# Kernel optimization log

Hardware: AMD Instinct MI355X
Metric: run time of the kernel (lower is better)

Reference implementation:

```python
import jax, jax.numpy as jnp
import numpy as np


def setup_inputs() -> dict:
    key = jax.random.key(0)
    k1, k2, k3 = jax.random.split(key, 3)
    B, C, T = 8, 256, 4096
    H, K = 512, 4
    x = jax.random.normal(k1, (B, C, T), dtype=jnp.float32)
    W = jax.random.normal(k2, (H, C * K), dtype=jnp.float32) * 0.02
    b = jax.random.normal(k3, (H,), dtype=jnp.float32) * 0.02
    return {"x": x, "W": W, "b": b}


def reference(x, W, b):
    # Causal conv1d equivalent of the per-step Linear loop (stride=1).
    # Original flattens window as view(B, C*K): channel-major -> W[h, c*K + k].
    B, C, T = x.shape
    H = W.shape[0]
    K = W.shape[1] // C
    kernel = W.reshape(H, C, K)  # OIH layout
    out = jax.lax.conv_general_dilated(
        x, kernel,
        window_strides=(1,),
        padding=[(K - 1, 0)],  # left-pad only => causal
        dimension_numbers=("NCH", "OIH", "NCH"),
    )
    return out + b[None, :, None]  # (B, H, T)
```

## Files before the change

kernel.cpp:

```cpp
#include <hip/hip_runtime.h>
#include <hip/hip_bf16.h>


#define Bb 8
#define Cc 256
#define Tt 4096
#define Hh 512
#define Kk 4

typedef __attribute__((ext_vector_type(8))) short bf16x8;
typedef __attribute__((ext_vector_type(4))) float f32x4;

#define WS_XT_OFF   0
#define WS_WT_OFF   16777216
#define WS_ZERO_OFF 17825792
#define WS_NEEDED   17826816ULL

__device__ __forceinline__ void gload16(const void* g, void* l) {
    __builtin_amdgcn_global_load_lds(
        (const __attribute__((address_space(1))) void*)g,
        (__attribute__((address_space(3))) void*)l, 16, 0, 0);
}

__global__ __launch_bounds__(256) void prep_kernel(const float* __restrict__ x,
                                                   const float* __restrict__ W,
                                                   __hip_bfloat16* __restrict__ xT,
                                                   __hip_bfloat16* __restrict__ Wt,
                                                   float* __restrict__ zeros) {
    __shared__ __hip_bfloat16 tile[64][72];
    const int bid = blockIdx.x;
    if (bid < 2048) {
        const int t0 = (bid & 63) * 64, c0 = ((bid >> 6) & 3) * 64, b = bid >> 8;
        const int lt = threadIdx.x & 63, lw = threadIdx.x >> 6;
#pragma unroll
        for (int i = 0; i < 16; ++i) {
            int cc = lw + i * 4;
            tile[cc][lt] = __float2bfloat16(x[((size_t)(b * Cc + c0 + cc)) * Tt + t0 + lt]);
        }
        __syncthreads();
#pragma unroll
        for (int i = 0; i < 2; ++i) {
            int tt = (threadIdx.x >> 3) + i * 32;
            int c8 = threadIdx.x & 7;
            short tmp[8];
#pragma unroll
            for (int j = 0; j < 8; ++j) {
                __hip_bfloat16 v = tile[c8 * 8 + j][tt];
                tmp[j] = *reinterpret_cast<short*>(&v);
            }
            *reinterpret_cast<bf16x8*>(&xT[((size_t)(b * Tt + t0 + tt)) * Cc + c0 + c8 * 8]) =
                *reinterpret_cast<bf16x8*>(tmp);
        }
    } else {
        int n = (bid - 2048) * 256 + threadIdx.x;
        int c = n & 255;
        int h = (n >> 8) & 511;
        int k = n >> 17;
        Wt[n] = __float2bfloat16(W[h * (Cc * Kk) + c * Kk + k]);
        if (bid == 2048) zeros[threadIdx.x] = 0.f;
    }
}

#define A_BUF    16384
#define B_BUF    9216
#define B_BASE   32768
#define LDS_TOTAL 51200

#define BAR __builtin_amdgcn_s_barrier()
#define LGKM0 do { asm volatile("s_waitcnt lgkmcnt(0)" ::: "memory"); \
                   __builtin_amdgcn_sched_barrier(0); } while (0)

__global__ __launch_bounds__(256, 3) void conv_mfma_kernel(
    const __hip_bfloat16* __restrict__ xT,
    const __hip_bfloat16* __restrict__ Wt,
    const float* __restrict__ bias,
    const float* __restrict__ zeros,
    float* __restrict__ out)
{
    __shared__ __align__(1024) char smem[LDS_TOTAL];
    const int tid = threadIdx.x, lane = tid & 63, wave = tid >> 6;
    const int wr = wave >> 1, wc = wave & 1;
    const int l15 = lane & 15, lg = lane >> 4;

    const int flat = blockIdx.x + 32 * blockIdx.y + 128 * blockIdx.z;
    const int nf   = (flat & 7) * 128 + (flat >> 3);
    const int h0 = (nf & 3) * 128;
    const int t0 = ((nf >> 2) & 31) * 128;
    const int b  = nf >> 7;

    const char* Wt_c = (const char*)Wt;
    const char* xT_c = (const char*)xT;
    const char* zz   = (const char*)zeros;

    const char* asrc[4]; int adst_[4];
#pragma unroll
    for (int i = 0; i < 4; ++i) {
        int s = tid + i * 256;
        int kk = s >> 9, row = (s >> 2) & 127, sl = s & 3;
        int colch = (sl ^ ((row >> 1) & 3)) * 8;
        asrc[i] = Wt_c + (((size_t)(kk * Hh + h0 + row)) * Cc + colch) * 2;
        adst_[i] = s * 16;
    }
    const char* bsrc[3]; int bdst_[3]; int bstep[3];
#pragma unroll
    for (int i = 0; i < 3; ++i) {
        int s = (i < 2) ? tid + i * 256 : 512 + lane;
        int row = s >> 2, sl = s & 3;
        int colch = (sl ^ ((row >> 1) & 3)) * 8;
        int tg = t0 - 3 + row;
        bool valid = (row <= 130) && (tg >= 0);
        bsrc[i]  = valid ? xT_c + (((size_t)b * Tt + tg) * Cc + colch) * 2
                         : zz + (s & 15) * 16;
        bstep[i] = valid ? 64 : 0;
        bdst_[i] = s * 16;
    }

    const int aoffb = (wr * 64 + l15) * 64 + ((lg ^ ((l15 >> 1) & 3)) << 4);
    int btab[4];
#pragma unroll
    for (int k = 0; k < 4; ++k)
        btab[k] = (wc * 64 + l15 + k) * 64 + ((lg ^ (((l15 + k) >> 1) & 3)) << 4);

    f32x4 acc[4][4] = {};

#pragma unroll
    for (int i = 0; i < 4; ++i) gload16(asrc[i], smem + adst_[i]);
#pragma unroll
    for (int i = 0; i < 2; ++i) gload16(bsrc[i], smem + B_BASE + bdst_[i]);
    if (wave == 0) gload16(bsrc[2], smem + B_BASE + bdst_[2]);
    asm volatile("s_waitcnt vmcnt(0)" ::: "memory");
    BAR;

#pragma unroll
    for (int s = 0; s < 16; ++s) {
        const int p  = s >> 1;
        const int kb = 2 * (s & 1);
        const char* Ab = smem + (s & 1) * A_BUF;
        const char* Bbf = smem + B_BASE + (p & 1) * B_BUF;

        if (s < 15) {
            const long aadv = (long)((s + 1) & 1) * 524288 + (long)((s + 1) >> 1) * 64;
            char* An = smem + ((s + 1) & 1) * A_BUF;
#pragma unroll
            for (int i = 0; i < 4; ++i) gload16(asrc[i] + aadv, An + adst_[i]);
        }
        if (((s & 1) == 0) && (p < 7)) {
            char* Bn = smem + B_BASE + ((p + 1) & 1) * B_BUF;
#pragma unroll
            for (int i = 0; i < 2; ++i) gload16(bsrc[i] + (p + 1) * bstep[i], Bn + bdst_[i]);
            if (wave == 0) gload16(bsrc[2] + (p + 1) * bstep[2], Bn + bdst_[2]);
        }

        bf16x8 a_[4], b_[4];
#pragma unroll
        for (int fm = 0; fm < 4; ++fm) a_[fm] = *(const bf16x8*)(Ab + aoffb + fm * 1024);
#pragma unroll
        for (int ft = 0; ft < 4; ++ft) b_[ft] = *(const bf16x8*)(Bbf + btab[kb] + ft * 1024);
        LGKM0;
        __builtin_amdgcn_s_setprio(1);
#pragma unroll
        for (int fm = 0; fm < 4; ++fm)
#pragma unroll
            for (int ft = 0; ft < 4; ++ft)
                acc[fm][ft] = __builtin_amdgcn_mfma_f32_16x16x32_bf16(a_[fm], b_[ft], acc[fm][ft], 0, 0, 0);
        __builtin_amdgcn_s_setprio(0);
#pragma unroll
        for (int fm = 0; fm < 4; ++fm) a_[fm] = *(const bf16x8*)(Ab + 8192 + aoffb + fm * 1024);
#pragma unroll
        for (int ft = 0; ft < 4; ++ft) b_[ft] = *(const bf16x8*)(Bbf + btab[kb + 1] + ft * 1024);
        LGKM0;
        __builtin_amdgcn_s_setprio(1);
#pragma unroll
        for (int fm = 0; fm < 4; ++fm)
#pragma unroll
            for (int ft = 0; ft < 4; ++ft)
                acc[fm][ft] = __builtin_amdgcn_mfma_f32_16x16x32_bf16(a_[fm], b_[ft], acc[fm][ft], 0, 0, 0);
        __builtin_amdgcn_s_setprio(0);

        if (s < 15) {
            if (((s & 1) == 0) && (p < 7)) asm volatile("s_waitcnt vmcnt(3)" ::: "memory");
            else                           asm volatile("s_waitcnt vmcnt(0)" ::: "memory");
            BAR;
        }
    }

#pragma unroll
    for (int fm = 0; fm < 4; ++fm) {
        int hb = h0 + wr * 64 + fm * 16 + lg * 4;
        float4 bs = *(const float4*)&bias[hb];
        const float* bsp = (const float*)&bs;
#pragma unroll
        for (int q = 0; q < 4; ++q)
#pragma unroll
            for (int ft = 0; ft < 4; ++ft) {
                int t = t0 + wc * 64 + ft * 16 + l15;
                out[((size_t)(b * Hh + hb + q)) * Tt + t] = acc[fm][ft][q] + bsp[q];
            }
    }
}

#define TT 256
#define HT 8
#define CT 4
__global__ __launch_bounds__(256) void conv1d_f32_kernel(
    const float* __restrict__ x, const float* __restrict__ W,
    const float* __restrict__ bias, float* __restrict__ out)
{
    const int tid = threadIdx.x;
    const int t0 = blockIdx.x * TT;
    const int h0 = blockIdx.y * HT;
    const int b  = blockIdx.z;
    __shared__ float xs[CT][TT + Kk];
    float acc[HT];
#pragma unroll
    for (int h = 0; h < HT; ++h) acc[h] = 0.f;
    const float* xb = x + (size_t)b * Cc * Tt;
    for (int c0 = 0; c0 < Cc; c0 += CT) {
        __syncthreads();
#pragma unroll
        for (int cc = 0; cc < CT; ++cc)
            for (int j = tid; j < TT + Kk - 1; j += 256) {
                int idx = t0 - (Kk - 1) + j;
                xs[cc][j] = (idx >= 0) ? xb[(size_t)(c0 + cc) * Tt + idx] : 0.f;
            }
        __syncthreads();
#pragma unroll
        for (int cc = 0; cc < CT; ++cc) {
            float xv[Kk];
#pragma unroll
            for (int k = 0; k < Kk; ++k) xv[k] = xs[cc][tid + k];
#pragma unroll
            for (int h = 0; h < HT; ++h) {
                const float* wp = W + (size_t)(h0 + h) * (Cc * Kk) + (size_t)(c0 + cc) * Kk;
#pragma unroll
                for (int k = 0; k < Kk; ++k) acc[h] += wp[k] * xv[k];
            }
        }
    }
#pragma unroll
    for (int h = 0; h < HT; ++h)
        out[((size_t)b * Hh + (h0 + h)) * Tt + t0 + tid] = acc[h] + bias[h0 + h];
}

extern "C" void kernel_launch(void* const* d_in, const int* in_sizes, int n_in,
                              void* d_out, int out_size, void* d_ws, size_t ws_size,
                              hipStream_t stream) {
    const float* x    = (const float*)d_in[0];
    const float* W    = (const float*)d_in[1];
    const float* bias = (const float*)d_in[2];
    float* out        = (float*)d_out;

    if (ws_size >= WS_NEEDED) {
        __hip_bfloat16* xT = (__hip_bfloat16*)((char*)d_ws + WS_XT_OFF);
        __hip_bfloat16* Wt = (__hip_bfloat16*)((char*)d_ws + WS_WT_OFF);
        float* zeros       = (float*)((char*)d_ws + WS_ZERO_OFF);

        prep_kernel<<<dim3(4096), dim3(256), 0, stream>>>(x, W, xT, Wt, zeros);
        conv_mfma_kernel<<<dim3(32, 4, 8), dim3(256), 0, stream>>>(xT, Wt, bias, zeros, out);
    } else {
        conv1d_f32_kernel<<<dim3(Tt / TT, Hh / HT, Bb), dim3(256), 0, stream>>>(x, W, bias, out);
    }
}
```

Measured before the change: 49.91 us.

## Switch to 32x32x16 MFMA tiles and triple-buffer the weight tiles

The GEMM inner loop now uses 32x32x16 bf16 MFMA instructions with a 2x2 fragment grid per wave, replacing the 4x4 grid of 16x16x32 instructions. This cuts the number of LDS fragment reads per unit of math. The weight (A) operand moves from double to triple buffering in LDS so that loads are issued two stages ahead, with the vmcnt waits adjusted to match. The larger LDS footprint drops the occupancy target from 3 to 2 blocks per CU. The loop is only unrolled by 2, and all waves now issue the third B load, which duplicates a write to the same LDS addresses.

```diff
diff --git a/kernel.cpp b/kernel.cpp
--- a/kernel.cpp
+++ b/kernel.cpp
@@ -8,8 +8,8 @@
 #define Hh 512
 #define Kk 4
 
-typedef __attribute__((ext_vector_type(8))) short bf16x8;
-typedef __attribute__((ext_vector_type(4))) float f32x4;
+typedef __attribute__((ext_vector_type(8)))  short bf16x8;
+typedef __attribute__((ext_vector_type(16))) float f32x16;
 
 #define WS_XT_OFF   0
 #define WS_WT_OFF   16777216
@@ -63,14 +63,14 @@
 
 #define A_BUF    16384
 #define B_BUF    9216
-#define B_BASE   32768
-#define LDS_TOTAL 51200
+#define B_BASE   49152
+#define LDS_TOTAL 67584
 
 #define BAR __builtin_amdgcn_s_barrier()
 #define LGKM0 do { asm volatile("s_waitcnt lgkmcnt(0)" ::: "memory"); \
                    __builtin_amdgcn_sched_barrier(0); } while (0)
 
-__global__ __launch_bounds__(256, 3) void conv_mfma_kernel(
+__global__ __launch_bounds__(256, 2) void conv_mfma_kernel(
     const __hip_bfloat16* __restrict__ xT,
     const __hip_bfloat16* __restrict__ Wt,
     const float* __restrict__ bias,
@@ -80,7 +80,7 @@
     __shared__ __align__(1024) char smem[LDS_TOTAL];
     const int tid = threadIdx.x, lane = tid & 63, wave = tid >> 6;
     const int wr = wave >> 1, wc = wave & 1;
-    const int l15 = lane & 15, lg = lane >> 4;
+    const int l31 = lane & 31, lh = lane >> 5;
 
     const int flat = blockIdx.x + 32 * blockIdx.y + 128 * blockIdx.z;
     const int nf   = (flat & 7) * 128 + (flat >> 3);
@@ -115,88 +115,99 @@
         bdst_[i] = s * 16;
     }
 
-    const int aoffb = (wr * 64 + l15) * 64 + ((lg ^ ((l15 >> 1) & 3)) << 4);
-    int btab[4];
-#pragma unroll
-    for (int k = 0; k < 4; ++k)
-        btab[k] = (wc * 64 + l15 + k) * 64 + ((lg ^ (((l15 + k) >> 1) & 3)) << 4);
-
-    f32x4 acc[4][4] = {};
-
-#pragma unroll
-    for (int i = 0; i < 4; ++i) gload16(asrc[i], smem + adst_[i]);
-#pragma unroll
-    for (int i = 0; i < 2; ++i) gload16(bsrc[i], smem + B_BASE + bdst_[i]);
-    if (wave == 0) gload16(bsrc[2], smem + B_BASE + bdst_[2]);
-    asm volatile("s_waitcnt vmcnt(0)" ::: "memory");
+    int arow[2], aswz[2];
+#pragma unroll
+    for (int fm = 0; fm < 2; ++fm) {
+        int r = wr * 64 + fm * 32 + l31;
+        arow[fm] = r * 64; aswz[fm] = (r >> 1) & 3;
+    }
+    int brow[4][2], bswz[4][2];
+#pragma unroll
+    for (int ck = 0; ck < 4; ++ck)
+#pragma unroll
+        for (int ft = 0; ft < 2; ++ft) {
+            int r = wc * 64 + ft * 32 + l31 + ck;
+            brow[ck][ft] = r * 64; bswz[ck][ft] = (r >> 1) & 3;
+        }
+
+    f32x16 acc[2][2] = {};
+
+    int A0 = 0, A1 = A_BUF, A2 = 2 * A_BUF;
+    int Bc = B_BASE, Bn = B_BASE + B_BUF;
+
+#pragma unroll
+    for (int i = 0; i < 4; ++i) gload16(asrc[i], smem + A0 + adst_[i]);
+#pragma unroll
+    for (int i = 0; i < 3; ++i) gload16(bsrc[i], smem + Bc + bdst_[i]);
+#pragma unroll
+    for (int i = 0; i < 4; ++i) gload16(asrc[i] + 524288, smem + A1 + adst_[i]);
+    asm volatile("s_waitcnt vmcnt(4)" ::: "memory");
     BAR;
 
-#pragma unroll
+#pragma unroll 2
     for (int s = 0; s < 16; ++s) {
-        const int p  = s >> 1;
-        const int kb = 2 * (s & 1);
-        const char* Ab = smem + (s & 1) * A_BUF;
-        const char* Bbf = smem + B_BASE + (p & 1) * B_BUF;
+        const int kb = (s & 1) * 2;
+
+        if (s <= 13) {
+            const long aadv = (long)((s + 2) & 1) * 524288 + (long)((s + 2) >> 1) * 64;
+#pragma unroll
+            for (int i = 0; i < 4; ++i) gload16(asrc[i] + aadv, smem + A2 + adst_[i]);
+        }
+        if (((s & 1) == 0) && (s <= 12)) {
+            const int bu = (s >> 1) + 1;
+#pragma unroll
+            for (int i = 0; i < 3; ++i) gload16(bsrc[i] + bu * bstep[i], smem + Bn + bdst_[i]);
+        }
+
+#pragma unroll
+        for (int kk = 0; kk < 2; ++kk) {
+            const int ck = kb + kk;
+            bf16x8 a_[2][2], b_[2][2];
+#pragma unroll
+            for (int sub = 0; sub < 2; ++sub) {
+#pragma unroll
+                for (int fm = 0; fm < 2; ++fm)
+                    a_[sub][fm] = *(const bf16x8*)(smem + A0 + kk * 8192 + arow[fm]
+                                    + (((sub * 2 + lh) ^ aswz[fm]) << 4));
+#pragma unroll
+                for (int ft = 0; ft < 2; ++ft)
+                    b_[sub][ft] = *(const bf16x8*)(smem + Bc + brow[ck][ft]
+                                    + (((sub * 2 + lh) ^ bswz[ck][ft]) << 4));
+            }
+            LGKM0;
+            __builtin_amdgcn_s_setprio(1);
+#pragma unroll
+            for (int sub = 0; sub < 2; ++sub)
+#pragma unroll
+                for (int fm = 0; fm < 2; ++fm)
+#pragma unroll
+                    for (int ft = 0; ft < 2; ++ft)
+                        acc[fm][ft] = __builtin_amdgcn_mfma_f32_32x32x16_bf16(
+                            a_[sub][fm], b_[sub][ft], acc[fm][ft], 0, 0, 0);
+            __builtin_amdgcn_s_setprio(0);
+        }
 
         if (s < 15) {
-            const long aadv = (long)((s + 1) & 1) * 524288 + (long)((s + 1) >> 1) * 64;
-            char* An = smem + ((s + 1) & 1) * A_BUF;
-#pragma unroll
-            for (int i = 0; i < 4; ++i) gload16(asrc[i] + aadv, An + adst_[i]);
-        }
-        if (((s & 1) == 0) && (p < 7)) {
-            char* Bn = smem + B_BASE + ((p + 1) & 1) * B_BUF;
-#pragma unroll
-            for (int i = 0; i < 2; ++i) gload16(bsrc[i] + (p + 1) * bstep[i], Bn + bdst_[i]);
-            if (wave == 0) gload16(bsrc[2] + (p + 1) * bstep[2], Bn + bdst_[2]);
-        }
-
-        bf16x8 a_[4], b_[4];
-#pragma unroll
-        for (int fm = 0; fm < 4; ++fm) a_[fm] = *(const bf16x8*)(Ab + aoffb + fm * 1024);
-#pragma unroll
-        for (int ft = 0; ft < 4; ++ft) b_[ft] = *(const bf16x8*)(Bbf + btab[kb] + ft * 1024);
-        LGKM0;
-        __builtin_amdgcn_s_setprio(1);
-#pragma unroll
-        for (int fm = 0; fm < 4; ++fm)
-#pragma unroll
-            for (int ft = 0; ft < 4; ++ft)
-                acc[fm][ft] = __builtin_amdgcn_mfma_f32_16x16x32_bf16(a_[fm], b_[ft], acc[fm][ft], 0, 0, 0);
-        __builtin_amdgcn_s_setprio(0);
-#pragma unroll
-        for (int fm = 0; fm < 4; ++fm) a_[fm] = *(const bf16x8*)(Ab + 8192 + aoffb + fm * 1024);
-#pragma unroll
-        for (int ft = 0; ft < 4; ++ft) b_[ft] = *(const bf16x8*)(Bbf + btab[kb + 1] + ft * 1024);
-        LGKM0;
-        __builtin_amdgcn_s_setprio(1);
-#pragma unroll
-        for (int fm = 0; fm < 4; ++fm)
-#pragma unroll
-            for (int ft = 0; ft < 4; ++ft)
-                acc[fm][ft] = __builtin_amdgcn_mfma_f32_16x16x32_bf16(a_[fm], b_[ft], acc[fm][ft], 0, 0, 0);
-        __builtin_amdgcn_s_setprio(0);
-
-        if (s < 15) {
-            if (((s & 1) == 0) && (p < 7)) asm volatile("s_waitcnt vmcnt(3)" ::: "memory");
-            else                           asm volatile("s_waitcnt vmcnt(0)" ::: "memory");
+            if (s & 1)          asm volatile("s_waitcnt vmcnt(4)" ::: "memory");
+            else if (s <= 12)   asm volatile("s_waitcnt vmcnt(7)" ::: "memory");
+            else                asm volatile("s_waitcnt vmcnt(0)" ::: "memory");
             BAR;
         }
-    }
-
-#pragma unroll
-    for (int fm = 0; fm < 4; ++fm) {
-        int hb = h0 + wr * 64 + fm * 16 + lg * 4;
-        float4 bs = *(const float4*)&bias[hb];
-        const float* bsp = (const float*)&bs;
-#pragma unroll
-        for (int q = 0; q < 4; ++q)
-#pragma unroll
-            for (int ft = 0; ft < 4; ++ft) {
-                int t = t0 + wc * 64 + ft * 16 + l15;
-                out[((size_t)(b * Hh + hb + q)) * Tt + t] = acc[fm][ft][q] + bsp[q];
-            }
-    }
+        int t_ = A0; A0 = A1; A1 = A2; A2 = t_;
+        if (s & 1) { int u_ = Bc; Bc = Bn; Bn = u_; }
+    }
+
+#pragma unroll
+    for (int fm = 0; fm < 2; ++fm)
+#pragma unroll
+        for (int ft = 0; ft < 2; ++ft)
+#pragma unroll
+            for (int r = 0; r < 16; ++r) {
+                int hl = (r & 3) + 8 * (r >> 2) + 4 * lh;
+                int h  = h0 + wr * 64 + fm * 32 + hl;
+                int t  = t0 + wc * 64 + ft * 32 + l31;
+                out[((size_t)(b * Hh + h)) * Tt + t] = acc[fm][ft][r] + bias[h];
+            }
 }
 
 #define TT 256
```

Result: slower. 57.37 us (+15.0%).
